# Kernel tuning notes

Measured on AMD Instinct MI355X. Metric: run time of the kernel, lower is better.

## Reference

```python
import jax, jax.numpy as jnp
from jax import lax
import numpy as np

B, T, I, H, OUT = 4096, 168, 4, 64, 12


def setup_inputs() -> dict:
    key = jax.random.key(0)
    ks = jax.random.split(key, 14)
    s = 0.05
    return {
        "x": jax.random.normal(ks[0], (B, T, I), dtype=jnp.float32),
        # LSTM layer 0 (PyTorch gate order: i, f, g, o)
        "Wih0": jax.random.normal(ks[1], (4 * H, I), dtype=jnp.float32) * s,
        "Whh0": jax.random.normal(ks[2], (4 * H, H), dtype=jnp.float32) * s,
        "bih0": jax.random.normal(ks[3], (4 * H,), dtype=jnp.float32) * s,
        "bhh0": jax.random.normal(ks[4], (4 * H,), dtype=jnp.float32) * s,
        # LSTM layer 1
        "Wih1": jax.random.normal(ks[5], (4 * H, H), dtype=jnp.float32) * s,
        "Whh1": jax.random.normal(ks[6], (4 * H, H), dtype=jnp.float32) * s,
        "bih1": jax.random.normal(ks[7], (4 * H,), dtype=jnp.float32) * s,
        "bhh1": jax.random.normal(ks[8], (4 * H,), dtype=jnp.float32) * s,
        # FC head: Linear(64,64) -> ReLU -> Linear(64,12)
        "W1": jax.random.normal(ks[9], (64, H), dtype=jnp.float32) * s,
        "b1": jax.random.normal(ks[10], (64,), dtype=jnp.float32) * s,
        "W2": jax.random.normal(ks[11], (OUT, 64), dtype=jnp.float32) * s,
        "b2": jax.random.normal(ks[12], (OUT,), dtype=jnp.float32) * s,
    }


def _lstm_layer(x, Wih, Whh, bih, bhh):
    # x: [B, T, in]; returns hidden sequence [B, T, H]
    Bsz = x.shape[0]
    Hd = Whh.shape[1]
    # Precompute input contribution for all timesteps: [B, T, 4H]
    xg = jnp.einsum('bti,gi->btg', x, Wih) + bih + bhh

    def step(carry, xg_t):
        h, c = carry
        g = xg_t + h @ Whh.T  # [B, 4H]
        i, f, gg, o = jnp.split(g, 4, axis=-1)
        i = jax.nn.sigmoid(i)
        f = jax.nn.sigmoid(f)
        gg = jnp.tanh(gg)
        o = jax.nn.sigmoid(o)
        c = f * c + i * gg
        h = o * jnp.tanh(c)
        return (h, c), h

    h0 = jnp.zeros((Bsz, Hd), x.dtype)
    (_, _), hs = lax.scan(step, (h0, h0), jnp.swapaxes(xg, 0, 1))  # hs: [T, B, H]
    return jnp.swapaxes(hs, 0, 1)


def reference(x, Wih0, Whh0, bih0, bhh0, Wih1, Whh1, bih1, bhh1, W1, b1, W2, b2):
    # Eval-mode forward: dropout layers are identity.
    h1 = _lstm_layer(x, Wih0, Whh0, bih0, bhh0)   # [B, T, H]
    h2 = _lstm_layer(h1, Wih1, Whh1, bih1, bhh1)  # [B, T, H]
    last = h2[:, -1, :]                            # [B, H]
    z = jax.nn.relu(last @ W1.T + b1)              # [B, 64]
    out = z @ W2.T + b2                            # [B, 12]
    return out.reshape(-1, 3, 4)
```

## Files before the change

### kernel.cpp

```cpp
#include <hip/hip_runtime.h>


typedef _Float16 h8 __attribute__((ext_vector_type(8)));
typedef _Float16 h4 __attribute__((ext_vector_type(4)));
typedef float f4 __attribute__((ext_vector_type(4)));

#define ROWB 208
#define HBUF (16 * ROWB)
#define H0_OFF 0
#define H1_OFF (2 * HBUF)
#define SMEM_TOTAL (4 * HBUF)

#define K1F 1.4426950408889634f
#define K2F 2.8853900817779268f

__device__ __forceinline__ float exp2_(float x) {
#if __has_builtin(__builtin_amdgcn_exp2f)
  return __builtin_amdgcn_exp2f(x);
#else
  float r; asm("v_exp_f32 %0, %1" : "=v"(r) : "v"(x)); return r;
#endif
}
__device__ __forceinline__ float rcp_(float x) {
#if __has_builtin(__builtin_amdgcn_rcpf)
  return __builtin_amdgcn_rcpf(x);
#else
  float r; asm("v_rcp_f32 %0, %1" : "=v"(r) : "v"(x)); return r;
#endif
}
__device__ __forceinline__ float sigmp(float a) { return rcp_(1.f + exp2_(-a)); }
__device__ __forceinline__ float tanhp(float a) { return 1.f - 2.f * rcp_(exp2_(a) + 1.f); }

__device__ __forceinline__ f4 mfma16(h8 a, h8 b, f4 c) {
  return __builtin_amdgcn_mfma_f32_16x16x32_f16(a, b, c, 0, 0, 0);
}

__device__ __forceinline__ h8 load_w8s(const float* __restrict__ p, float sc) {
  h8 r;
#pragma unroll
  for (int j = 0; j < 8; j++) r[j] = (_Float16)(p[j] * sc);
  return r;
}

__device__ __forceinline__ unsigned packh2(float a, float b) {
  unsigned lo = (unsigned)__builtin_bit_cast(unsigned short, (_Float16)a);
  unsigned hi = (unsigned)__builtin_bit_cast(unsigned short, (_Float16)b);
  return lo | (hi << 16);
}

extern "C" __global__ void __launch_bounds__(512, 2)
weather_lstm_mfma3(const float* __restrict__ x,
                   const float* __restrict__ Wih0, const float* __restrict__ Whh0,
                   const float* __restrict__ bih0, const float* __restrict__ bhh0,
                   const float* __restrict__ Wih1, const float* __restrict__ Whh1,
                   const float* __restrict__ bih1, const float* __restrict__ bhh1,
                   const float* __restrict__ W1, const float* __restrict__ b1,
                   const float* __restrict__ W2, const float* __restrict__ b2,
                   float* __restrict__ out)
{
  __shared__ __align__(16) unsigned char smem[SMEM_TOTAL];
  const int tid  = threadIdx.x;
  const int lane = tid & 63;
  const int w    = tid >> 6;
  const int col  = lane & 15;
  const int quad = lane >> 4;
  const int sB   = blockIdx.x * 16;

  const int g_  = col & 3;
  const int ul_ = col >> 2;
  const float asc = (g_ == 2) ? K2F : K1F;
  int arow[2];
  arow[0] = g_ * 64 + w * 8 + 2 * ul_ + 0;
  arow[1] = g_ * 64 + w * 8 + 2 * ul_ + 1;

  h8 a0[2][3], a1i[2][2], a1h[2][2];
#pragma unroll
  for (int T = 0; T < 2; T++) {
    const int r = arow[T];
#pragma unroll
    for (int f = 0; f < 2; f++) {
      a0[T][f]  = load_w8s(Whh0 + r * 64 + f * 32 + quad * 8, asc);
      a1i[T][f] = load_w8s(Wih1 + r * 64 + f * 32 + quad * 8, asc);
      a1h[T][f] = load_w8s(Whh1 + r * 64 + f * 32 + quad * 8, asc);
    }
    h8 xw = {};
    if (quad == 0) {
#pragma unroll
      for (int j = 0; j < 4; j++) xw[j] = (_Float16)(Wih0[r * 4 + j] * asc);
    }
    a0[T][2] = xw;
  }

  f4 bias0v[2], bias1v[2];
#pragma unroll
  for (int T = 0; T < 2; T++) {
#pragma unroll
    for (int reg = 0; reg < 4; reg++) {
      const int rr = reg * 64 + w * 8 + 2 * quad + T;
      const float bs = (reg == 2) ? K2F : K1F;
      bias0v[T][reg] = (bih0[rr] + bhh0[rr]) * bs;
      bias1v[T][reg] = (bih1[rr] + bhh1[rr]) * bs;
    }
  }

  for (int idx = tid; idx < SMEM_TOTAL / 4; idx += 512) ((int*)smem)[idx] = 0;
  __syncthreads();
  if (tid < 16) {
    f4 xv = *(const f4*)(x + ((size_t)(sB + tid) * 168 + 0) * 4);
    h4 xh;
#pragma unroll
    for (int j = 0; j < 4; j++) xh[j] = (_Float16)xv[j];
    *(h4*)(smem + H0_OFF + 0 * HBUF + tid * ROWB + 128) = xh;
  }
  __syncthreads();

  float c0[2] = {0.f, 0.f}, c1[2] = {0.f, 0.f};
  float hl[2] = {0.f, 0.f};
  const int bo = col * ROWB + quad * 16;
  const int wo = col * ROWB + (w * 8 + 2 * quad) * 2;

  for (int t = 0; t < 168; t++) {
    const int pb = t & 1, nb = pb ^ 1;
    unsigned char* h0p = smem + H0_OFF + pb * HBUF;
    unsigned char* h0n = smem + H0_OFF + nb * HBUF;
    unsigned char* h1p = smem + H1_OFF + pb * HBUF;
    unsigned char* h1n = smem + H1_OFF + nb * HBUF;

    if (tid < 16) {
      const int tn = (t < 167) ? t + 1 : 167;
      f4 xv = *(const f4*)(x + ((size_t)(sB + tid) * 168 + tn) * 4);
      h4 xh;
#pragma unroll
      for (int j = 0; j < 4; j++) xh[j] = (_Float16)xv[j];
      *(h4*)(h0n + tid * ROWB + 128) = xh;
    }

    h8 b0  = *(const h8*)(h0p + bo);
    h8 b1v = *(const h8*)(h0p + bo + 64);
    h8 b2v = *(const h8*)(h0p + bo + 128);
    h8 q0  = *(const h8*)(h1p + bo);
    h8 q1  = *(const h8*)(h1p + bo + 64);

    f4 l1a0 = mfma16(a1h[0][0], q0, bias1v[0]);
    f4 l1a1 = mfma16(a1h[1][0], q0, bias1v[1]);
    l1a0 = mfma16(a1h[0][1], q1, l1a0);
    l1a1 = mfma16(a1h[1][1], q1, l1a1);

    f4 acc0 = mfma16(a0[0][0], b0, bias0v[0]);
    f4 acc1 = mfma16(a0[1][0], b0, bias0v[1]);
    acc0 = mfma16(a0[0][1], b1v, acc0);
    acc1 = mfma16(a0[1][1], b1v, acc1);
    acc0 = mfma16(a0[0][2], b2v, acc0);
    acc1 = mfma16(a0[1][2], b2v, acc1);

    float h0o[2];
#pragma unroll
    for (int T = 0; T < 2; T++) {
      f4 a = T ? acc1 : acc0;
      float iv = sigmp(a[0]);
      float fv = sigmp(a[1]);
      float gv = tanhp(a[2]);
      float ov = sigmp(a[3]);
      c0[T] = fv * c0[T] + iv * gv;
      h0o[T] = ov * tanhp(c0[T] * K2F);
    }
    *(unsigned*)(h0n + wo) = packh2(h0o[0], h0o[1]);
    __syncthreads();

    h8 p0 = *(const h8*)(h0n + bo);
    h8 p1 = *(const h8*)(h0n + bo + 64);
    l1a0 = mfma16(a1i[0][0], p0, l1a0);
    l1a1 = mfma16(a1i[1][0], p0, l1a1);
    l1a0 = mfma16(a1i[0][1], p1, l1a0);
    l1a1 = mfma16(a1i[1][1], p1, l1a1);

#pragma unroll
    for (int T = 0; T < 2; T++) {
      f4 a = T ? l1a1 : l1a0;
      float iv = sigmp(a[0]);
      float fv = sigmp(a[1]);
      float gv = tanhp(a[2]);
      float ov = sigmp(a[3]);
      c1[T] = fv * c1[T] + iv * gv;
      hl[T] = ov * tanhp(c1[T] * K2F);
    }
    *(unsigned*)(h1n + wo) = packh2(hl[0], hl[1]);
    __syncthreads();
  }

  float* fh = (float*)smem;
#pragma unroll
  for (int T = 0; T < 2; T++)
    fh[col * 64 + (w * 8 + 2 * quad + T)] = hl[T];
  __syncthreads();

  {
    const int u = tid & 63, grp = tid >> 6;
    float za0 = b1[u], za1 = b1[u];
    const float* w1r = W1 + u * 64;
    const float* f0 = fh + (grp * 2 + 0) * 64;
    const float* f1 = fh + (grp * 2 + 1) * 64;
    for (int j = 0; j < 64; j++) {
      float wv = w1r[j];
      za0 += wv * f0[j];
      za1 += wv * f1[j];
    }
    float* zl = (float*)(smem + 4096);
    zl[(grp * 2 + 0) * 64 + u] = fmaxf(za0, 0.f);
    zl[(grp * 2 + 1) * 64 + u] = fmaxf(za1, 0.f);
  }
  __syncthreads();

  if (tid < 192) {
    const float* zl = (const float*)(smem + 4096);
    const int s = tid / 12, o = tid - s * 12;
    float a = b2[o];
    for (int j = 0; j < 64; j++) a += W2[o * 64 + j] * zl[s * 64 + j];
    out[(sB + s) * 12 + o] = a;
  }
}

extern "C" void kernel_launch(void* const* d_in, const int* in_sizes, int n_in,
                              void* d_out, int out_size, void* d_ws, size_t ws_size,
                              hipStream_t stream) {
  (void)in_sizes; (void)n_in; (void)d_ws; (void)ws_size; (void)out_size;
  const float* x    = (const float*)d_in[0];
  const float* Wih0 = (const float*)d_in[1];
  const float* Whh0 = (const float*)d_in[2];
  const float* bih0 = (const float*)d_in[3];
  const float* bhh0 = (const float*)d_in[4];
  const float* Wih1 = (const float*)d_in[5];
  const float* Whh1 = (const float*)d_in[6];
  const float* bih1 = (const float*)d_in[7];
  const float* bhh1 = (const float*)d_in[8];
  const float* W1   = (const float*)d_in[9];
  const float* b1   = (const float*)d_in[10];
  const float* W2   = (const float*)d_in[11];
  const float* b2   = (const float*)d_in[12];

  weather_lstm_mfma3<<<dim3(256), dim3(512), 0, stream>>>(
      x, Wih0, Whh0, bih0, bhh0, Wih1, Whh1, bih1, bhh1, W1, b1, W2, b2,
      (float*)d_out);
}
```

Before: 233.3 us.

## Skew two LSTM layers into one wavefront step and preload x into LDS

Layer 1 now runs one timestep behind layer 0 inside the same loop iteration, so each step needs a single barrier instead of two, and all MFMAs for both layers are issued together. The whole x sequence for the block is converted to fp16 and staged in LDS up front, which removes the per-step global loads. The gate activations are rewritten to share one reciprocal across the four gates. The costs are about 43KB of extra LDS and launch bounds lowered to one block per CU, plus possible precision loss from multiplying four denominators together.

```diff
diff --git a/kernel.cpp b/kernel.cpp
--- a/kernel.cpp
+++ b/kernel.cpp
@@ -7,9 +7,11 @@
 
 #define ROWB 208
 #define HBUF (16 * ROWB)
-#define H0_OFF 0
-#define H1_OFF (2 * HBUF)
-#define SMEM_TOTAL (4 * HBUF)
+#define XTAB_OFF 0
+#define XTAB_BYTES (169 * 256)
+#define H0_OFF XTAB_BYTES
+#define H1_OFF (H0_OFF + 2 * HBUF)
+#define SMEM_TOTAL (H1_OFF + 2 * HBUF)
 
 #define K1F 1.4426950408889634f
 #define K2F 2.8853900817779268f
@@ -28,8 +30,6 @@
   float r; asm("v_rcp_f32 %0, %1" : "=v"(r) : "v"(x)); return r;
 #endif
 }
-__device__ __forceinline__ float sigmp(float a) { return rcp_(1.f + exp2_(-a)); }
-__device__ __forceinline__ float tanhp(float a) { return 1.f - 2.f * rcp_(exp2_(a) + 1.f); }
 
 __device__ __forceinline__ f4 mfma16(h8 a, h8 b, f4 c) {
   return __builtin_amdgcn_mfma_f32_16x16x32_f16(a, b, c, 0, 0, 0);
@@ -48,8 +48,25 @@
   return lo | (hi << 16);
 }
 
-extern "C" __global__ void __launch_bounds__(512, 2)
-weather_lstm_mfma3(const float* __restrict__ x,
+__device__ __forceinline__ void lstm_act(f4 a, float& c, float& h) {
+  float Ei = exp2_(-a[0]);
+  float Ef = exp2_(-a[1]);
+  float Eg = exp2_(a[2]);
+  float Eo = exp2_(-a[3]);
+  float A = 1.f + Ei, B = 1.f + Ef, C = 1.f + Eg, D = 1.f + Eo;
+  float AB = A * B, CD = C * D;
+  float R = rcp_(AB * CD);
+  float iv = (B * CD) * R;
+  float fv = (A * CD) * R;
+  float gv = 1.f - 2.f * ((AB * D) * R);
+  float ov = (AB * C) * R;
+  c = fv * c + iv * gv;
+  float Ec = exp2_(c * K2F);
+  h = ov * (1.f - 2.f * rcp_(Ec + 1.f));
+}
+
+extern "C" __global__ void __launch_bounds__(512, 1)
+weather_lstm_mfma4(const float* __restrict__ x,
                    const float* __restrict__ Wih0, const float* __restrict__ Whh0,
                    const float* __restrict__ bih0, const float* __restrict__ bhh0,
                    const float* __restrict__ Wih1, const float* __restrict__ Whh1,
@@ -105,12 +122,13 @@
 
   for (int idx = tid; idx < SMEM_TOTAL / 4; idx += 512) ((int*)smem)[idx] = 0;
   __syncthreads();
-  if (tid < 16) {
-    f4 xv = *(const f4*)(x + ((size_t)(sB + tid) * 168 + 0) * 4);
+  for (int idx = tid; idx < 16 * 168; idx += 512) {
+    const int c_ = idx / 168, t_ = idx - c_ * 168;
+    f4 xv = *(const f4*)(x + ((size_t)(sB + c_) * 168 + t_) * 4);
     h4 xh;
 #pragma unroll
     for (int j = 0; j < 4; j++) xh[j] = (_Float16)xv[j];
-    *(h4*)(smem + H0_OFF + 0 * HBUF + tid * ROWB + 128) = xh;
+    *(h4*)(smem + XTAB_OFF + t_ * 256 + c_ * 16) = xh;
   }
   __syncthreads();
 
@@ -118,73 +136,47 @@
   float hl[2] = {0.f, 0.f};
   const int bo = col * ROWB + quad * 16;
   const int wo = col * ROWB + (w * 8 + 2 * quad) * 2;
-
-  for (int t = 0; t < 168; t++) {
-    const int pb = t & 1, nb = pb ^ 1;
-    unsigned char* h0p = smem + H0_OFF + pb * HBUF;
-    unsigned char* h0n = smem + H0_OFF + nb * HBUF;
-    unsigned char* h1p = smem + H1_OFF + pb * HBUF;
-    unsigned char* h1n = smem + H1_OFF + nb * HBUF;
-
-    if (tid < 16) {
-      const int tn = (t < 167) ? t + 1 : 167;
-      f4 xv = *(const f4*)(x + ((size_t)(sB + tid) * 168 + tn) * 4);
-      h4 xh;
-#pragma unroll
-      for (int j = 0; j < 4; j++) xh[j] = (_Float16)xv[j];
-      *(h4*)(h0n + tid * ROWB + 128) = xh;
-    }
-
-    h8 b0  = *(const h8*)(h0p + bo);
-    h8 b1v = *(const h8*)(h0p + bo + 64);
-    h8 b2v = *(const h8*)(h0p + bo + 128);
-    h8 q0  = *(const h8*)(h1p + bo);
-    h8 q1  = *(const h8*)(h1p + bo + 64);
-
-    f4 l1a0 = mfma16(a1h[0][0], q0, bias1v[0]);
-    f4 l1a1 = mfma16(a1h[1][0], q0, bias1v[1]);
-    l1a0 = mfma16(a1h[0][1], q1, l1a0);
-    l1a1 = mfma16(a1h[1][1], q1, l1a1);
-
-    f4 acc0 = mfma16(a0[0][0], b0, bias0v[0]);
-    f4 acc1 = mfma16(a0[1][0], b0, bias0v[1]);
-    acc0 = mfma16(a0[0][1], b1v, acc0);
-    acc1 = mfma16(a0[1][1], b1v, acc1);
-    acc0 = mfma16(a0[0][2], b2v, acc0);
-    acc1 = mfma16(a0[1][2], b2v, acc1);
-
-    float h0o[2];
-#pragma unroll
-    for (int T = 0; T < 2; T++) {
-      f4 a = T ? acc1 : acc0;
-      float iv = sigmp(a[0]);
-      float fv = sigmp(a[1]);
-      float gv = tanhp(a[2]);
-      float ov = sigmp(a[3]);
-      c0[T] = fv * c0[T] + iv * gv;
-      h0o[T] = ov * tanhp(c0[T] * K2F);
-    }
-    *(unsigned*)(h0n + wo) = packh2(h0o[0], h0o[1]);
-    __syncthreads();
-
-    h8 p0 = *(const h8*)(h0n + bo);
-    h8 p1 = *(const h8*)(h0n + bo + 64);
-    l1a0 = mfma16(a1i[0][0], p0, l1a0);
-    l1a1 = mfma16(a1i[1][0], p0, l1a1);
-    l1a0 = mfma16(a1i[0][1], p1, l1a0);
-    l1a1 = mfma16(a1i[1][1], p1, l1a1);
-
-#pragma unroll
-    for (int T = 0; T < 2; T++) {
-      f4 a = T ? l1a1 : l1a0;
-      float iv = sigmp(a[0]);
-      float fv = sigmp(a[1]);
-      float gv = tanhp(a[2]);
-      float ov = sigmp(a[3]);
-      c1[T] = fv * c1[T] + iv * gv;
-      hl[T] = ov * tanhp(c1[T] * K2F);
-    }
-    *(unsigned*)(h1n + wo) = packh2(hl[0], hl[1]);
+  const unsigned char* xp = smem + XTAB_OFF + col * 16;
+
+  for (int k = 0; k <= 168; k++) {
+    const int kb = k & 1, kbn = kb ^ 1;
+    const unsigned char* h0r = smem + H0_OFF + kbn * HBUF;
+    unsigned char*       h0w = smem + H0_OFF + kb  * HBUF;
+    const unsigned char* h1r = smem + H1_OFF + kb  * HBUF;
+    unsigned char*       h1w = smem + H1_OFF + kbn * HBUF;
+
+    h8 b0  = *(const h8*)(h0r + bo);
+    h8 b1v = *(const h8*)(h0r + bo + 64);
+    h8 bx  = *(const h8*)(xp + k * 256);
+    h8 q0  = *(const h8*)(h1r + bo);
+    h8 q1  = *(const h8*)(h1r + bo + 64);
+
+    f4 A0 = mfma16(a0[0][0], b0, bias0v[0]);
+    f4 A1 = mfma16(a0[1][0], b0, bias0v[1]);
+    f4 C0 = mfma16(a1i[0][0], b0, bias1v[0]);
+    f4 C1 = mfma16(a1i[1][0], b0, bias1v[1]);
+    A0 = mfma16(a0[0][1], b1v, A0);
+    A1 = mfma16(a0[1][1], b1v, A1);
+    C0 = mfma16(a1i[0][1], b1v, C0);
+    C1 = mfma16(a1i[1][1], b1v, C1);
+    A0 = mfma16(a0[0][2], bx, A0);
+    A1 = mfma16(a0[1][2], bx, A1);
+    C0 = mfma16(a1h[0][0], q0, C0);
+    C1 = mfma16(a1h[1][0], q0, C1);
+    C0 = mfma16(a1h[0][1], q1, C0);
+    C1 = mfma16(a1h[1][1], q1, C1);
+
+    if (k < 168) {
+      float h0o[2];
+      lstm_act(A0, c0[0], h0o[0]);
+      lstm_act(A1, c0[1], h0o[1]);
+      *(unsigned*)(h0w + wo) = packh2(h0o[0], h0o[1]);
+    }
+    if (k > 0) {
+      lstm_act(C0, c1[0], hl[0]);
+      lstm_act(C1, c1[1], hl[1]);
+      *(unsigned*)(h1w + wo) = packh2(hl[0], hl[1]);
+    }
     __syncthreads();
   }
 
@@ -238,7 +230,7 @@
   const float* W2   = (const float*)d_in[11];
   const float* b2   = (const float*)d_in[12];
 
-  weather_lstm_mfma3<<<dim3(256), dim3(512), 0, stream>>>(
+  weather_lstm_mfma4<<<dim3(256), dim3(512), 0, stream>>>(
       x, Wih0, Whh0, bih0, bhh0, Wih1, Whh1, bih1, bhh1, W1, b1, W2, b2,
       (float*)d_out);
 }
```

Result: faster. 227.0 us (-2.7%).
